# Kernel tuning notes

Hardware: AMD Instinct MI355X
Metric: run time of the kernel (lower is better)

The kernel has to match this reference:

```python
import jax, jax.numpy as jnp
import numpy as np

IN_SIZE = 512
HID = 512
BATCH = 65536


def setup_inputs() -> dict:
    key = jax.random.key(0)
    ks = jax.random.split(key, 20)
    s = 1.0 / np.sqrt(IN_SIZE)
    sh = 1.0 / np.sqrt(HID)
    d = {
        "inputs": jax.random.normal(ks[0], (BATCH, IN_SIZE), jnp.float32),
        "state": jax.random.normal(ks[1], (BATCH, HID), jnp.float32),
        "parent_state": jax.random.normal(ks[2], (BATCH, HID), jnp.float32),
    }
    # input-path linears (with bias), torch Linear layout: W [out, in], y = x @ W.T + b
    for i, name in enumerate(["w_a", "w_r", "w_r1", "w_c"]):
        d[name + "_w"] = jax.random.uniform(ks[3 + 2 * i], (HID, IN_SIZE), jnp.float32, -s, s)
        d[name + "_b"] = jax.random.uniform(ks[4 + 2 * i], (HID,), jnp.float32, -s, s)
    # state-path and parent-path linears (no bias)
    for i, name in enumerate(["u_a", "u_r", "u_r1", "u_c", "p_a", "p_r", "p_r1", "p_c"]):
        d[name + "_w"] = jax.random.uniform(ks[11 + i], (HID, HID), jnp.float32, -sh, sh)
    return d


def reference(inputs, state, parent_state,
              w_a_w, w_a_b, w_r_w, w_r_b, w_r1_w, w_r1_b, w_c_w, w_c_b,
              u_a_w, u_r_w, u_r1_w, u_c_w,
              p_a_w, p_r_w, p_r1_w, p_c_w):
    def lin(x, w, b=None):
        y = x @ w.T
        return y if b is None else y + b

    att = jax.nn.sigmoid(lin(inputs, w_a_w, w_a_b) + lin(state, u_a_w) + lin(parent_state, p_a_w))
    r = jax.nn.sigmoid(lin(inputs, w_r_w, w_r_b) + lin(state, u_r_w) + lin(parent_state, p_r_w))
    r1 = jax.nn.sigmoid(lin(inputs, w_r1_w, w_r1_b) + lin(state, u_r1_w) + lin(parent_state, p_r1_w))
    c = jnp.tanh(lin(inputs, w_c_w, w_c_b) + lin(state * r, u_c_w) + lin(parent_state * r1, p_c_w))
    new_h = att * c + (1.0 - att) * state
    return new_h
```

## Files before the change

kernel.cpp:

```cpp
#include <hip/hip_runtime.h>
#include <stdint.h>


typedef unsigned short u16;
using bf16x8 = __attribute__((ext_vector_type(8))) __bf16;
using f32x4  = __attribute__((ext_vector_type(4))) float;

__device__ __forceinline__ u16 f2bf(float f) {
    __bf16 b = (__bf16)f;
    union { __bf16 b; u16 u; } v; v.b = b;
    return v.u;
}
__device__ __forceinline__ uint32_t f2bf2(float lo, float hi) {
    return (uint32_t)f2bf(lo) | ((uint32_t)f2bf(hi) << 16);
}
__device__ __forceinline__ float bf2f(u16 s) {
    union { uint32_t u; float f; } v; v.u = ((uint32_t)s) << 16;
    return v.f;
}
__device__ __forceinline__ void load_lds16(const void* g, void* l) {
    __builtin_amdgcn_global_load_lds(
        (const __attribute__((address_space(1))) uint32_t*)g,
        (__attribute__((address_space(3))) uint32_t*)l, 16, 0, 0);
}

__global__ void prep_weights(
    const float* __restrict__ wa, const float* __restrict__ ua, const float* __restrict__ pa,
    const float* __restrict__ wrg, const float* __restrict__ ur, const float* __restrict__ pr,
    const float* __restrict__ wr1, const float* __restrict__ ur1, const float* __restrict__ pr1,
    const float* __restrict__ wcc, const float* __restrict__ uc, const float* __restrict__ pc,
    u16* __restrict__ B1, u16* __restrict__ B2)
{
    int idx = blockIdx.x * 256 + threadIdx.x;
    const int T1 = 1536 * 1536;
    if (idx < T1) {
        int n = idx / 1536, k = idx - n * 1536;
        int g = n >> 9, nn = n & 511;
        int o = k >> 9, kk = k & 511;
        const float* s;
        if (g == 0)      s = (o == 0) ? wa  : (o == 1) ? ua  : pa;
        else if (g == 1) s = (o == 0) ? wrg : (o == 1) ? ur  : pr;
        else             s = (o == 0) ? wr1 : (o == 1) ? ur1 : pr1;
        B1[idx] = f2bf(s[nn * 512 + kk]);
    } else {
        int j = idx - T1;
        if (j < 512 * 1536) {
            int n = j / 1536, k = j - n * 1536;
            int o = k >> 9, kk = k & 511;
            const float* s = (o == 0) ? wcc : (o == 1) ? uc : pc;
            B2[j] = f2bf(s[n * 512 + kk]);
        }
    }
}

__global__ void cast_inputs(const float* __restrict__ X, const float* __restrict__ H,
                            const float* __restrict__ P,
                            u16* __restrict__ Xb, u16* __restrict__ Hb, u16* __restrict__ Pb)
{
    const long long MAT8 = (65536LL * 512) / 8;
    for (long long t = (long long)blockIdx.x * 256 + threadIdx.x;
         t < 3 * MAT8; t += (long long)gridDim.x * 256) {
        int m = (int)(t >> 22);
        long long e = (t & (MAT8 - 1)) * 8;
        const float* s = (m == 0) ? X : (m == 1) ? H : P;
        u16* d = (m == 0) ? Xb : (m == 1) ? Hb : Pb;
        f32x4 a = *(const f32x4*)(s + e);
        f32x4 b = *(const f32x4*)(s + e + 4);
        uint4 q;
        q.x = f2bf2(a.x, a.y); q.y = f2bf2(a.z, a.w);
        q.z = f2bf2(b.x, b.y); q.w = f2bf2(b.z, b.w);
        *(uint4*)(d + e) = q;
    }
}

template<int MODE>
__global__ __launch_bounds__(256, 4)
void g128(const u16* __restrict__ A0, const u16* __restrict__ A1s, const u16* __restrict__ A2s,
          const u16* __restrict__ Bw,
          const float* __restrict__ bias0, const float* __restrict__ bias1,
          const float* __restrict__ bias2,
          const u16* __restrict__ HbP, const u16* __restrict__ PbP,
          u16* __restrict__ attb, u16* __restrict__ hrw, u16* __restrict__ pr1w,
          float* __restrict__ outp)
{
    __shared__ u16 Ab[128 * 64];
    __shared__ u16 Bb[128 * 64];

    const int tid  = threadIdx.x;
    const int lane = tid & 63;
    const int w    = tid >> 6;
    const int wr   = w >> 1;
    const int wc   = w & 1;

    int panel, ntl;
    const int xcd = blockIdx.x & 7;
    const int idx = blockIdx.x >> 3;
    if (MODE == 1) { panel = xcd * 64 + idx / 12;   ntl = idx % 12; }
    else           { panel = xcd * 64 + (idx >> 2); ntl = idx & 3;  }
    const int m0 = panel * 128;
    const int n0 = ntl * 128;

    const int srow = w * 32 + (lane >> 3);
    const int scol = ((lane & 7) ^ (lane >> 3)) * 8;
    const int ofsA = srow * 512  + scol;
    const int ofsB = srow * 1536 + scol;
    const u16* const bA0 = A0  + (size_t)m0 * 512;
    const u16* const bA1 = A1s + (size_t)m0 * 512;
    const u16* const bA2 = A2s + (size_t)m0 * 512;
    const u16* const bB  = Bw  + (size_t)n0 * 1536;

    auto issueA = [&](int kt) {
        const u16* src = (kt < 8) ? bA0 : (kt < 16) ? bA1 : bA2;
        const u16* g = src + (kt & 7) * 64 + ofsA;
        u16* lb = &Ab[(w * 32) * 64];
#pragma unroll
        for (int c = 0; c < 4; ++c)
            load_lds16(g + c * 8 * 512, lb + c * 8 * 64);
    };
    auto issueB = [&](int kt) {
        const u16* g = bB + kt * 64 + ofsB;
        u16* lb = &Bb[(w * 32) * 64];
#pragma unroll
        for (int c = 0; c < 4; ++c)
            load_lds16(g + c * 8 * 1536, lb + c * 8 * 64);
    };

    f32x4 acc[4][4];
    const f32x4 vz = {0.0f, 0.0f, 0.0f, 0.0f};
#pragma unroll
    for (int i = 0; i < 4; ++i)
#pragma unroll
        for (int j = 0; j < 4; ++j) acc[i][j] = vz;

    auto compute = [&]() {
        const int rsw = (lane & 7) << 3;
        const int rb  = lane & 15;
        const int hi8 = (lane >> 4) * 8;
#pragma unroll
        for (int ks = 0; ks < 2; ++ks) {
            bf16x8 af[4], bfr[4];
            const int col = (ks * 32 + hi8) ^ rsw;
#pragma unroll
            for (int fm = 0; fm < 4; ++fm)
                af[fm] = *(const bf16x8*)&Ab[(wr * 64 + fm * 16 + rb) * 64 + col];
#pragma unroll
            for (int fn = 0; fn < 4; ++fn)
                bfr[fn] = *(const bf16x8*)&Bb[(wc * 64 + fn * 16 + rb) * 64 + col];
#pragma unroll
            for (int fm = 0; fm < 4; ++fm)
#pragma unroll
                for (int fn = 0; fn < 4; ++fn)
                    acc[fm][fn] = __builtin_amdgcn_mfma_f32_16x16x32_bf16(
                        af[fm], bfr[fn], acc[fm][fn], 0, 0, 0);
        }
    };

#pragma unroll 1
    for (int kt = 0; kt < 24; ++kt) {
        issueA(kt); issueB(kt);
        __syncthreads();
        compute();
        __syncthreads();
    }

    const int rl = (lane >> 4) * 4;
    const int cl = lane & 15;
    const int rb0 = m0 + wr * 64 + rl;
    if (MODE == 1) {
        const int gate = ntl >> 2;
        const float* bias = (gate == 0) ? bias0 : (gate == 1) ? bias1 : bias2;
        const int nnb = (ntl & 3) * 128 + wc * 64;
#pragma unroll
        for (int fm = 0; fm < 4; ++fm)
#pragma unroll
            for (int fn = 0; fn < 4; ++fn) {
                const int nn = nnb + fn * 16 + cl;
                const float b = bias[nn];
                int off = (rb0 + fm * 16) * 512 + nn;
#pragma unroll
                for (int j = 0; j < 4; ++j, off += 512) {
                    float v = acc[fm][fn][j] + b;
                    float s = 1.0f / (1.0f + __expf(-v));
                    if (gate == 0)      attb[off] = f2bf(s);
                    else if (gate == 1) hrw[off]  = f2bf(s * bf2f(HbP[off]));
                    else                pr1w[off] = f2bf(s * bf2f(PbP[off]));
                }
            }
    } else {
        const int nnb = n0 + wc * 64;
#pragma unroll
        for (int fm = 0; fm < 4; ++fm)
#pragma unroll
            for (int fn = 0; fn < 4; ++fn) {
                const int nn = nnb + fn * 16 + cl;
                const float b = bias0[nn];
                int off = (rb0 + fm * 16) * 512 + nn;
#pragma unroll
                for (int j = 0; j < 4; ++j, off += 512) {
                    float v = acc[fm][fn][j] + b;
                    float e = __expf(2.0f * v);
                    float ct = 1.0f - 2.0f / (e + 1.0f);
                    float a = bf2f(attb[off]);
                    float h = bf2f(HbP[off]);
                    outp[off] = a * ct + (1.0f - a) * h;
                }
            }
    }
}

__global__ __launch_bounds__(256, 2)
void k1_small(const float* __restrict__ X, const float* __restrict__ H,
              const float* __restrict__ P, const u16* __restrict__ B1,
              const float* __restrict__ ba, const float* __restrict__ br,
              const float* __restrict__ br1,
              float* __restrict__ attf, u16* __restrict__ hrw, u16* __restrict__ pr1w)
{
    __shared__ u16 Ab[2][128 * 64];
    __shared__ u16 Bb[2][128 * 64];
    const int tid = threadIdx.x, lane = tid & 63, w = tid >> 6;
    const int wr = w >> 1, wc = w & 1;
    const int bid = blockIdx.x, xcd = bid & 7, idx = bid >> 3;
    const int panel = idx / 12, ntl = idx - panel * 12;
    const int m0 = (xcd * 64 + panel) * 128, n0 = ntl * 128;
    const int srow = w * 32 + (lane >> 3);
    const int scol = ((lane & 7) ^ (lane >> 3)) * 8;
    const int arow = tid >> 4, acol = (tid & 15) * 4;
    const int aswz = acol ^ ((arow & 7) << 3);
    f32x4 acc[4][4];
    const f32x4 vz = {0, 0, 0, 0};
#pragma unroll
    for (int i = 0; i < 4; ++i)
#pragma unroll
        for (int j = 0; j < 4; ++j) acc[i][j] = vz;
    f32x4 areg[8];
    auto issueA = [&](int kt) {
        const float* src = (kt < 8) ? X : (kt < 16) ? H : P;
        const float* base = src + (size_t)(m0 + arow) * 512 + (kt & 7) * 64 + acol;
#pragma unroll
        for (int rr = 0; rr < 8; ++rr)
            areg[rr] = *(const f32x4*)(base + (size_t)(rr * 16) * 512);
    };
    auto writeA = [&](int nb) {
#pragma unroll
        for (int rr = 0; rr < 8; ++rr) {
            uint2 q; q.x = f2bf2(areg[rr].x, areg[rr].y);
            q.y = f2bf2(areg[rr].z, areg[rr].w);
            *(uint2*)&Ab[nb][(arow + rr * 16) * 64 + aswz] = q;
        }
    };
    auto issueB = [&](int kt, int nb) {
        const u16* gb = B1 + (size_t)(n0 + srow) * 1536 + kt * 64 + scol;
        u16* lb = &Bb[nb][(w * 32) * 64];
#pragma unroll
        for (int c = 0; c < 4; ++c)
            load_lds16(gb + (size_t)c * 8 * 1536, lb + c * 8 * 64);
    };
    auto compute = [&](int cb) {
        const int rsw = (lane & 7) << 3, rb = lane & 15, hi8 = (lane >> 4) * 8;
#pragma unroll
        for (int ks = 0; ks < 2; ++ks) {
            bf16x8 af[4], bfr[4];
            const int col = (ks * 32 + hi8) ^ rsw;
#pragma unroll
            for (int fm = 0; fm < 4; ++fm)
                af[fm] = *(const bf16x8*)&Ab[cb][(wr * 64 + fm * 16 + rb) * 64 + col];
#pragma unroll
            for (int fn = 0; fn < 4; ++fn)
                bfr[fn] = *(const bf16x8*)&Bb[cb][(wc * 64 + fn * 16 + rb) * 64 + col];
#pragma unroll
            for (int fm = 0; fm < 4; ++fm)
#pragma unroll
                for (int fn = 0; fn < 4; ++fn)
                    acc[fm][fn] = __builtin_amdgcn_mfma_f32_16x16x32_bf16(
                        af[fm], bfr[fn], acc[fm][fn], 0, 0, 0);
        }
    };
    issueA(0); issueB(0, 0); writeA(0);
    __syncthreads();
    int cb = 0;
#pragma unroll 2
    for (int kt = 0; kt < 24; ++kt) {
        if (kt < 23) { issueA(kt + 1); issueB(kt + 1, cb ^ 1); }
        compute(cb);
        if (kt < 23) writeA(cb ^ 1);
        __syncthreads();
        cb ^= 1;
    }
    const int gate = ntl >> 2;
    const float* bias = (gate == 0) ? ba : (gate == 1) ? br : br1;
    const int nnb = (ntl & 3) * 128 + wc * 64;
    const int rl = (lane >> 4) * 4, cl = lane & 15;
#pragma unroll
    for (int fm = 0; fm < 4; ++fm)
#pragma unroll
        for (int fn = 0; fn < 4; ++fn) {
            const int nn = nnb + fn * 16 + cl;
            const float b = bias[nn];
#pragma unroll
            for (int j = 0; j < 4; ++j) {
                const int row = m0 + wr * 64 + fm * 16 + rl + j;
                const size_t off = (size_t)row * 512 + nn;
                float v = acc[fm][fn][j] + b;
                float s = 1.0f / (1.0f + __expf(-v));
                if (gate == 0)      attf[off] = s;
                else if (gate == 1) hrw[off]  = f2bf(s * H[off]);
                else                pr1w[off] = f2bf(s * P[off]);
            }
        }
}

__global__ __launch_bounds__(256, 2)
void k2_small(const float* __restrict__ X, const float* __restrict__ H,
              const u16* __restrict__ B2, const float* __restrict__ bc,
              const u16* __restrict__ hrw, const u16* __restrict__ pr1w,
              float* outp)
{
    __shared__ u16 Ab[2][128 * 64];
    __shared__ u16 Bb[2][128 * 64];
    const int tid = threadIdx.x, lane = tid & 63, w = tid >> 6;
    const int wr = w >> 1, wc = w & 1;
    const int bid = blockIdx.x, xcd = bid & 7, idx = bid >> 3;
    const int panel = idx >> 2, ntl = idx & 3;
    const int m0 = (xcd * 64 + panel) * 128, n0 = ntl * 128;
    const int srow = w * 32 + (lane >> 3);
    const int scol = ((lane & 7) ^ (lane >> 3)) * 8;
    const int arow = tid >> 4, acol = (tid & 15) * 4;
    const int aswz = acol ^ ((arow & 7) << 3);
    f32x4 acc[4][4];
    const f32x4 vz = {0, 0, 0, 0};
#pragma unroll
    for (int i = 0; i < 4; ++i)
#pragma unroll
        for (int j = 0; j < 4; ++j) acc[i][j] = vz;
    f32x4 areg[8];
    auto issueA = [&](int kt, int nb) {
        if (kt >= 8) {
            const u16* src = (kt < 16) ? hrw : pr1w;
            const u16* gb = src + (size_t)(m0 + srow) * 512 + (kt & 7) * 64 + scol;
            u16* lb = &Ab[nb][(w * 32) * 64];
#pragma unroll
            for (int c = 0; c < 4; ++c)
                load_lds16(gb + (size_t)c * 8 * 512, lb + c * 8 * 64);
        } else {
            const float* base = X + (size_t)(m0 + arow) * 512 + (kt & 7) * 64 + acol;
#pragma unroll
            for (int rr = 0; rr < 8; ++rr)
                areg[rr] = *(const f32x4*)(base + (size_t)(rr * 16) * 512);
        }
    };
    auto writeA = [&](int kt, int nb) {
        if (kt < 8) {
#pragma unroll
            for (int rr = 0; rr < 8; ++rr) {
                uint2 q; q.x = f2bf2(areg[rr].x, areg[rr].y);
                q.y = f2bf2(areg[rr].z, areg[rr].w);
                *(uint2*)&Ab[nb][(arow + rr * 16) * 64 + aswz] = q;
            }
        }
    };
    auto issueB = [&](int kt, int nb) {
        const u16* gb = B2 + (size_t)(n0 + srow) * 1536 + kt * 64 + scol;
        u16* lb = &Bb[nb][(w * 32) * 64];
#pragma unroll
        for (int c = 0; c < 4; ++c)
            load_lds16(gb + (size_t)c * 8 * 1536, lb + c * 8 * 64);
    };
    auto compute = [&](int cb) {
        const int rsw = (lane & 7) << 3, rb = lane & 15, hi8 = (lane >> 4) * 8;
#pragma unroll
        for (int ks = 0; ks < 2; ++ks) {
            bf16x8 af[4], bfr[4];
            const int col = (ks * 32 + hi8) ^ rsw;
#pragma unroll
            for (int fm = 0; fm < 4; ++fm)
                af[fm] = *(const bf16x8*)&Ab[cb][(wr * 64 + fm * 16 + rb) * 64 + col];
#pragma unroll
            for (int fn = 0; fn < 4; ++fn)
                bfr[fn] = *(const bf16x8*)&Bb[cb][(wc * 64 + fn * 16 + rb) * 64 + col];
#pragma unroll
            for (int fm = 0; fm < 4; ++fm)
#pragma unroll
                for (int fn = 0; fn < 4; ++fn)
                    acc[fm][fn] = __builtin_amdgcn_mfma_f32_16x16x32_bf16(
                        af[fm], bfr[fn], acc[fm][fn], 0, 0, 0);
        }
    };
    issueA(0, 0); issueB(0, 0); writeA(0, 0);
    __syncthreads();
    int cb = 0;
#pragma unroll 2
    for (int kt = 0; kt < 24; ++kt) {
        if (kt < 23) { issueA(kt + 1, cb ^ 1); issueB(kt + 1, cb ^ 1); }
        compute(cb);
        if (kt < 23) writeA(kt + 1, cb ^ 1);
        __syncthreads();
        cb ^= 1;
    }
    const int nnb = n0 + wc * 64;
    const int rl = (lane >> 4) * 4, cl = lane & 15;
#pragma unroll
    for (int fm = 0; fm < 4; ++fm)
#pragma unroll
        for (int fn = 0; fn < 4; ++fn) {
            const int nn = nnb + fn * 16 + cl;
            const float b = bc[nn];
#pragma unroll
            for (int j = 0; j < 4; ++j) {
                const int row = m0 + wr * 64 + fm * 16 + rl + j;
                const size_t off = (size_t)row * 512 + nn;
                float v = acc[fm][fn][j] + b;
                float e = __expf(2.0f * v);
                float ct = 1.0f - 2.0f / (e + 1.0f);
                float a = outp[off];
                outp[off] = a * ct + (1.0f - a) * H[off];
            }
        }
}

extern "C" void kernel_launch(void* const* d_in, const int* in_sizes, int n_in,
                              void* d_out, int out_size, void* d_ws, size_t ws_size,
                              hipStream_t stream)
{
    const float* X   = (const float*)d_in[0];
    const float* H   = (const float*)d_in[1];
    const float* P   = (const float*)d_in[2];
    const float* wa  = (const float*)d_in[3];
    const float* ba  = (const float*)d_in[4];
    const float* wrg = (const float*)d_in[5];
    const float* br  = (const float*)d_in[6];
    const float* wr1 = (const float*)d_in[7];
    const float* br1 = (const float*)d_in[8];
    const float* wcc = (const float*)d_in[9];
    const float* bc  = (const float*)d_in[10];
    const float* ua  = (const float*)d_in[11];
    const float* ur  = (const float*)d_in[12];
    const float* ur1 = (const float*)d_in[13];
    const float* uc  = (const float*)d_in[14];
    const float* pa  = (const float*)d_in[15];
    const float* pr  = (const float*)d_in[16];
    const float* pr1 = (const float*)d_in[17];
    const float* pc  = (const float*)d_in[18];

    char* ws = (char*)d_ws;
    u16* B1   = (u16*)(ws);
    u16* B2   = (u16*)(ws + (size_t)4718592);
    u16* hrp  = (u16*)(ws + (size_t)6291456);
    u16* pr1p = (u16*)(ws + (size_t)73400320);
    u16* Xb   = (u16*)(ws + (size_t)140509184);
    u16* Hb   = (u16*)(ws + (size_t)207618048);
    u16* Pb   = (u16*)(ws + (size_t)274726912);
    u16* attb = (u16*)(ws + (size_t)341835776);
    float* out = (float*)d_out;

    const bool big3 = ws_size >= (size_t)408944640ULL;

    prep_weights<<<12288, 256, 0, stream>>>(wa, ua, pa, wrg, ur, pr, wr1, ur1, pr1,
                                            wcc, uc, pc, B1, B2);
    if (big3) {
        cast_inputs<<<3072, 256, 0, stream>>>(X, H, P, Xb, Hb, Pb);
        g128<1><<<6144, 256, 0, stream>>>(Xb, Hb, Pb, B1, ba, br, br1,
                                          Hb, Pb, attb, hrp, pr1p, out);
        g128<2><<<2048, 256, 0, stream>>>(Xb, hrp, pr1p, B2, bc, nullptr, nullptr,
                                          Hb, nullptr, attb, nullptr, nullptr, out);
    } else {
        k1_small<<<6144, 256, 0, stream>>>(X, H, P, B1, ba, br, br1, out, hrp, pr1p);
        k2_small<<<2048, 256, 0, stream>>>(X, H, B2, bc, hrp, pr1p, out);
    }
}
```

Baseline: 726.2 us.

## Double-buffer LDS tiles with BK=32 to overlap global loads with MFMA

Splits the K tile from 64 to 32 and adds two LDS buffers for A and B, so the global-to-LDS load for the next step is issued before computing on the current buffer. This removes one barrier per iteration and overlaps memory latency with MFMA work. It doubles the iteration count with half the work each, changes the swizzle pattern, and keeps LDS use the same. There is a risk that waitcnt handling around the direct-to-LDS loads serialises anyway.

```diff
diff --git a/kernel.cpp b/kernel.cpp
--- a/kernel.cpp
+++ b/kernel.cpp
@@ -83,8 +83,8 @@
           u16* __restrict__ attb, u16* __restrict__ hrw, u16* __restrict__ pr1w,
           float* __restrict__ outp)
 {
-    __shared__ u16 Ab[128 * 64];
-    __shared__ u16 Bb[128 * 64];
+    __shared__ u16 Ab[2][128 * 32];
+    __shared__ u16 Bb[2][128 * 32];
 
     const int tid  = threadIdx.x;
     const int lane = tid & 63;
@@ -100,29 +100,29 @@
     const int m0 = panel * 128;
     const int n0 = ntl * 128;
 
-    const int srow = w * 32 + (lane >> 3);
-    const int scol = ((lane & 7) ^ (lane >> 3)) * 8;
-    const int ofsA = srow * 512  + scol;
-    const int ofsB = srow * 1536 + scol;
+    const int srow = tid >> 2;
+    const int sgrp = tid & 3;
+    const int sg2  = (sgrp ^ ((srow >> 1) & 3)) * 8;
+    const int ofsA = srow * 512  + sg2;
+    const int ofsB = srow * 1536 + sg2;
     const u16* const bA0 = A0  + (size_t)m0 * 512;
     const u16* const bA1 = A1s + (size_t)m0 * 512;
     const u16* const bA2 = A2s + (size_t)m0 * 512;
     const u16* const bB  = Bw  + (size_t)n0 * 1536;
-
-    auto issueA = [&](int kt) {
-        const u16* src = (kt < 8) ? bA0 : (kt < 16) ? bA1 : bA2;
-        const u16* g = src + (kt & 7) * 64 + ofsA;
-        u16* lb = &Ab[(w * 32) * 64];
-#pragma unroll
-        for (int c = 0; c < 4; ++c)
-            load_lds16(g + c * 8 * 512, lb + c * 8 * 64);
-    };
-    auto issueB = [&](int kt) {
-        const u16* g = bB + kt * 64 + ofsB;
-        u16* lb = &Bb[(w * 32) * 64];
-#pragma unroll
-        for (int c = 0; c < 4; ++c)
-            load_lds16(g + c * 8 * 1536, lb + c * 8 * 64);
+    const int ldst = tid * 8;
+
+    auto stageA = [&](int kt, int nb) {
+        const u16* src = (kt < 16) ? bA0 : (kt < 32) ? bA1 : bA2;
+        const u16* g = src + (kt & 15) * 32 + ofsA;
+        u16* lb = &Ab[nb][ldst];
+        load_lds16(g,            lb);
+        load_lds16(g + 64 * 512, lb + 2048);
+    };
+    auto stageB = [&](int kt, int nb) {
+        const u16* g = bB + kt * 32 + ofsB;
+        u16* lb = &Bb[nb][ldst];
+        load_lds16(g,             lb);
+        load_lds16(g + 64 * 1536, lb + 2048);
     };
 
     f32x4 acc[4][4];
@@ -132,35 +132,36 @@
 #pragma unroll
         for (int j = 0; j < 4; ++j) acc[i][j] = vz;
 
-    auto compute = [&]() {
-        const int rsw = (lane & 7) << 3;
-        const int rb  = lane & 15;
-        const int hi8 = (lane >> 4) * 8;
-#pragma unroll
-        for (int ks = 0; ks < 2; ++ks) {
-            bf16x8 af[4], bfr[4];
-            const int col = (ks * 32 + hi8) ^ rsw;
-#pragma unroll
-            for (int fm = 0; fm < 4; ++fm)
-                af[fm] = *(const bf16x8*)&Ab[(wr * 64 + fm * 16 + rb) * 64 + col];
+    const int fr  = lane & 15;
+    const int cg  = (((lane >> 4) ^ ((fr >> 1) & 3))) * 8;
+    const int aOff = (wr * 64 + fr) * 32 + cg;
+    const int bOff = (wc * 64 + fr) * 32 + cg;
+
+    auto compute = [&](int cb) {
+        bf16x8 af[4], bfr[4];
+#pragma unroll
+        for (int fm = 0; fm < 4; ++fm)
+            af[fm] = *(const bf16x8*)&Ab[cb][aOff + fm * 512];
+#pragma unroll
+        for (int fn = 0; fn < 4; ++fn)
+            bfr[fn] = *(const bf16x8*)&Bb[cb][bOff + fn * 512];
+#pragma unroll
+        for (int fm = 0; fm < 4; ++fm)
 #pragma unroll
             for (int fn = 0; fn < 4; ++fn)
-                bfr[fn] = *(const bf16x8*)&Bb[(wc * 64 + fn * 16 + rb) * 64 + col];
-#pragma unroll
-            for (int fm = 0; fm < 4; ++fm)
-#pragma unroll
-                for (int fn = 0; fn < 4; ++fn)
-                    acc[fm][fn] = __builtin_amdgcn_mfma_f32_16x16x32_bf16(
-                        af[fm], bfr[fn], acc[fm][fn], 0, 0, 0);
-        }
-    };
-
+                acc[fm][fn] = __builtin_amdgcn_mfma_f32_16x16x32_bf16(
+                    af[fm], bfr[fn], acc[fm][fn], 0, 0, 0);
+    };
+
+    stageA(0, 0); stageB(0, 0);
+    __syncthreads();
+    int buf = 0;
 #pragma unroll 1
-    for (int kt = 0; kt < 24; ++kt) {
-        issueA(kt); issueB(kt);
+    for (int kt = 0; kt < 48; ++kt) {
+        if (kt < 47) { stageA(kt + 1, buf ^ 1); stageB(kt + 1, buf ^ 1); }
+        compute(buf);
         __syncthreads();
-        compute();
-        __syncthreads();
+        buf ^= 1;
     }
 
     const int rl = (lane >> 4) * 4;
```

Measured after the change: 804.8 us. 10.8% more time.
